# Kernel tuning notes

Hardware: AMD Instinct MI355X
Metric: run time of the kernel (lower is better)

The kernel has to match this reference:

```python
import jax, jax.numpy as jnp
import numpy as np

Q_MAX = 127.0  # int8 symmetric quant range


def setup_inputs() -> dict:
    key = jax.random.key(0)
    kx, kw, ks = jax.random.split(key, 3)
    M, K, N = 16384, 4096, 4096
    x = jax.random.normal(kx, (M, K), dtype=jnp.float32)
    # int8 weight values in [-127, 127]
    weight = jax.random.randint(kw, (N, K), -127, 128, dtype=jnp.int32).astype(jnp.int8)
    # per-output-row dequant scale, small positive values as a real quantizer would produce
    weight_scale = jax.random.uniform(ks, (N, 1), dtype=jnp.float32, minval=1e-3, maxval=1e-2)
    return {"x": x, "weight": weight, "weight_scale": weight_scale}


def reference(x, weight, weight_scale):
    # --- per-token dynamic activation quantization (get_hip_quant(per_Token)) ---
    amax = jnp.max(jnp.abs(x), axis=-1, keepdims=True)            # [M,1]
    x_scale = amax / Q_MAX                                        # [M,1]
    x_q = jnp.clip(jnp.round(x / jnp.maximum(x_scale, 1e-8)), -Q_MAX, Q_MAX)  # int8 values, kept fp32
    # --- gemm_a8w8: int8xint8 GEMM with fused dequant (row scale_a * col scale_b) ---
    acc = jnp.einsum('mk,nk->mn', x_q, weight.astype(jnp.float32),
                     preferred_element_type=jnp.float32)          # [M,N] int accumulation in fp32
    y = acc * x_scale * weight_scale.T                            # fused dequant scales
    return y  # fp32 stand-in for otype=bf16 output
```

## Files before the change

kernel.cpp:

```cpp
#include <hip/hip_runtime.h>
#include <stdint.h>

#define M_DIM 16384
#define N_DIM 4096
#define K_DIM 4096

#define BM 256
#define BN 256
#define BK 128
#define NT (K_DIM / BK)

typedef int i32x4 __attribute__((ext_vector_type(4)));

__device__ __forceinline__ void async16(const uint8_t* g, uint8_t* l) {
    __builtin_amdgcn_global_load_lds(
        (const __attribute__((address_space(1))) void*)g,
        (__attribute__((address_space(3))) void*)l,
        16, 0, 0);
}

__global__ __launch_bounds__(256) void pack_w_kernel(const int* __restrict__ w32,
                                                     uint32_t* __restrict__ w8,
                                                     int n4) {
    int i = blockIdx.x * 256 + threadIdx.x;
    if (i < n4) {
        const int4 v = reinterpret_cast<const int4*>(w32)[i];
        uint32_t p = (uint32_t)(v.x & 255) | ((uint32_t)(v.y & 255) << 8) |
                     ((uint32_t)(v.z & 255) << 16) | ((uint32_t)(v.w & 255) << 24);
        w8[i] = p;
    }
}

__global__ __launch_bounds__(256) void quant_kernel(const float* __restrict__ x,
                                                    uint32_t* __restrict__ xq,
                                                    float* __restrict__ xscale) {
    const int m = blockIdx.x;
    const int t = threadIdx.x;
    const float4* row = reinterpret_cast<const float4*>(x + (size_t)m * K_DIM);
    float4 v[4];
    float amax = 0.0f;
#pragma unroll
    for (int i = 0; i < 4; ++i) {
        v[i] = row[t + i * 256];
        amax = fmaxf(amax, fmaxf(fmaxf(fabsf(v[i].x), fabsf(v[i].y)),
                                 fmaxf(fabsf(v[i].z), fabsf(v[i].w))));
    }
#pragma unroll
    for (int off = 32; off > 0; off >>= 1) amax = fmaxf(amax, __shfl_xor(amax, off));
    __shared__ float smax[4];
    if ((t & 63) == 0) smax[t >> 6] = amax;
    __syncthreads();
    amax = fmaxf(fmaxf(smax[0], smax[1]), fmaxf(smax[2], smax[3]));
    const float scale = amax / 127.0f;
    const float s = fmaxf(scale, 1e-8f);
    if (t == 0) xscale[m] = scale;
    uint32_t* orow = xq + (size_t)m * (K_DIM / 4);
#pragma unroll
    for (int i = 0; i < 4; ++i) {
        int q0 = __float2int_rn(v[i].x / s);
        int q1 = __float2int_rn(v[i].y / s);
        int q2 = __float2int_rn(v[i].z / s);
        int q3 = __float2int_rn(v[i].w / s);
        q0 = max(-127, min(127, q0));
        q1 = max(-127, min(127, q1));
        q2 = max(-127, min(127, q2));
        q3 = max(-127, min(127, q3));
        uint32_t p = (uint32_t)(q0 & 255) | ((uint32_t)(q1 & 255) << 8) |
                     ((uint32_t)(q2 & 255) << 16) | ((uint32_t)(q3 & 255) << 24);
        orow[t + i * 256] = p;
    }
}

__global__ __launch_bounds__(512, 2) void gemm_kernel(
    const uint8_t* __restrict__ Aq, const float* __restrict__ ascale,
    const uint8_t* __restrict__ Bq, const float* __restrict__ wscale,
    float* __restrict__ out) {
    __shared__ uint8_t lds[2 * BM * BK + 2 * BN * BK];
    uint8_t* ldsA0 = lds;
    uint8_t* ldsA1 = lds + BM * BK;
    uint8_t* ldsB0 = lds + 2 * BM * BK;
    uint8_t* ldsB1 = lds + 2 * BM * BK + BN * BK;

    const int tid = threadIdx.x;
    const int lane = tid & 63;
    const int w = tid >> 6;
    const int wr = w >> 2;
    const int wc = w & 3;
    const int lr = lane & 15;
    const int lg = lane >> 4;
    const int aa = lane >> 3;
    const int pp = lane & 7;

    const int bid = blockIdx.x;
    const int swz = (bid & 7) * (1024 / 8) + (bid >> 3);
    const size_t row0 = (size_t)(swz >> 4) * BM;
    const size_t col0 = (size_t)(swz & 15) * BN;
    const uint8_t* Ab = Aq + row0 * K_DIM;
    const uint8_t* Bb = Bq + col0 * K_DIM;

    i32x4 acc[8][4];
#pragma unroll
    for (int i = 0; i < 8; ++i)
#pragma unroll
        for (int j = 0; j < 4; ++j) acc[i][j] = (i32x4){0, 0, 0, 0};

#define STAGE_A(DST, KT, MH)                                                     \
    do {                                                                         \
        _Pragma("unroll") for (int it_ = 0; it_ < 2; ++it_) {                    \
            const int m_ = (MH) * 64 + w * 8 + aa + it_ * 128;                   \
            async16(Ab + (size_t)m_ * K_DIM + (KT) * BK + ((pp ^ aa) << 4),      \
                    (DST) + ((MH) * 64 + w * 8 + it_ * 128) * BK);               \
        }                                                                        \
    } while (0)

#define STAGE_B(DST, KT, NH)                                                     \
    do {                                                                         \
        _Pragma("unroll") for (int it_ = 0; it_ < 2; ++it_) {                    \
            const int rwh_ = it_ * 64 + w * 8 + aa;                              \
            const int n_ = (NH) * 32 + (rwh_ & 31) + ((rwh_ >> 5) << 6);         \
            const int rw0_ = it_ * 64 + w * 8;                                   \
            const int nb_ = (NH) * 32 + (rw0_ & 31) + ((rw0_ >> 5) << 6);        \
            async16(Bb + (size_t)n_ * K_DIM + (KT) * BK + ((pp ^ aa) << 4),      \
                    (DST) + nb_ * BK);                                           \
        }                                                                        \
    } while (0)

#define READ_A(BUF, MH)                                                          \
    do {                                                                         \
        _Pragma("unroll") for (int mf_ = 0; mf_ < 4; ++mf_)                      \
        _Pragma("unroll") for (int kk_ = 0; kk_ < 2; ++kk_) {                    \
            const int r_ = wr * 128 + (MH) * 64 + mf_ * 16 + lr;                 \
            const int u_ = kk_ * 4 + lg;                                         \
            af[mf_][kk_] = *reinterpret_cast<const i32x4*>(                      \
                (BUF) + r_ * BK + ((u_ ^ (r_ & 7)) << 4));                       \
        }                                                                        \
    } while (0)

#define READ_B(BUF, NH, DSTF)                                                    \
    do {                                                                         \
        _Pragma("unroll") for (int nf_ = 0; nf_ < 2; ++nf_)                      \
        _Pragma("unroll") for (int kk_ = 0; kk_ < 2; ++kk_) {                    \
            const int r_ = wc * 64 + (NH) * 32 + nf_ * 16 + lr;                  \
            const int u_ = kk_ * 4 + lg;                                         \
            DSTF[nf_][kk_] = *reinterpret_cast<const i32x4*>(                    \
                (BUF) + r_ * BK + ((u_ ^ (r_ & 7)) << 4));                       \
        }                                                                        \
    } while (0)

#define MFMA_QUAD(MH, NH, BF)                                                    \
    do {                                                                         \
        __builtin_amdgcn_s_setprio(1);                                           \
        _Pragma("unroll") for (int mf_ = 0; mf_ < 4; ++mf_)                      \
        _Pragma("unroll") for (int nf_ = 0; nf_ < 2; ++nf_)                      \
        _Pragma("unroll") for (int kk_ = 0; kk_ < 2; ++kk_)                      \
            acc[(MH) * 4 + mf_][(NH) * 2 + nf_] =                                \
                __builtin_amdgcn_mfma_i32_16x16x64_i8(                           \
                    af[mf_][kk_], BF[nf_][kk_],                                  \
                    acc[(MH) * 4 + mf_][(NH) * 2 + nf_], 0, 0, 0);               \
        __builtin_amdgcn_s_setprio(0);                                           \
    } while (0)

#define BAR __builtin_amdgcn_s_barrier()
#define VMCNT6 asm volatile("s_waitcnt vmcnt(6)" ::: "memory")

    STAGE_A(ldsA0, 0, 0);
    STAGE_A(ldsA0, 0, 1);
    STAGE_B(ldsB0, 0, 0);
    STAGE_B(ldsB0, 0, 1);
    STAGE_A(ldsA1, 1, 0);
    STAGE_B(ldsB1, 1, 0);
    STAGE_B(ldsB1, 1, 1);
    VMCNT6;
    BAR;

    i32x4 af[4][2], bfA[2][2], bfB[2][2];

#pragma unroll 1
    for (int it2 = 0; it2 < NT / 2; ++it2) {
        const int t = 2 * it2;
        const int kt2 = (t + 2 < NT) ? t + 2 : NT - 1;
        const int kt3 = (t + 3 < NT) ? t + 3 : NT - 1;

        READ_A(ldsA0, 0);
        READ_B(ldsB0, 0, bfA);
        STAGE_A(ldsA1, t + 1, 1);
        BAR;
        MFMA_QUAD(0, 0, bfA);
        BAR;

        READ_B(ldsB0, 1, bfB);
        STAGE_A(ldsA0, kt2, 0);
        BAR;
        MFMA_QUAD(0, 1, bfB);
        BAR;

        READ_A(ldsA0, 1);
        STAGE_B(ldsB0, kt2, 0);
        BAR;
        MFMA_QUAD(1, 1, bfB);
        BAR;

        STAGE_B(ldsB0, kt2, 1);
        BAR;
        MFMA_QUAD(1, 0, bfA);
        VMCNT6;
        BAR;

        READ_A(ldsA1, 0);
        READ_B(ldsB1, 0, bfA);
        STAGE_A(ldsA0, kt2, 1);
        BAR;
        MFMA_QUAD(0, 0, bfA);
        BAR;

        READ_B(ldsB1, 1, bfB);
        STAGE_A(ldsA1, kt3, 0);
        BAR;
        MFMA_QUAD(0, 1, bfB);
        BAR;

        READ_A(ldsA1, 1);
        STAGE_B(ldsB1, kt3, 0);
        BAR;
        MFMA_QUAD(1, 1, bfB);
        BAR;

        STAGE_B(ldsB1, kt3, 1);
        BAR;
        MFMA_QUAD(1, 0, bfA);
        VMCNT6;
        BAR;
    }

    const float* asp = ascale + row0 + wr * 128;
    const float* wsp = wscale + col0 + wc * 64;
    float wsv[4];
#pragma unroll
    for (int nf = 0; nf < 4; ++nf) wsv[nf] = wsp[nf * 16 + lr];
    float* outBase = out + (row0 + wr * 128) * (size_t)N_DIM + col0 + wc * 64;
#pragma unroll
    for (int mf = 0; mf < 8; ++mf) {
#pragma unroll
        for (int j = 0; j < 4; ++j) {
            const int r = mf * 16 + lg * 4 + j;
            const float av = asp[r];
            float* orow = outBase + (size_t)r * N_DIM;
#pragma unroll
            for (int nf = 0; nf < 4; ++nf) {
                orow[nf * 16 + lr] = (float)acc[mf][nf][j] * av * wsv[nf];
            }
        }
    }
#undef STAGE_A
#undef STAGE_B
#undef READ_A
#undef READ_B
#undef MFMA_QUAD
#undef BAR
#undef VMCNT6
}

extern "C" void kernel_launch(void* const* d_in, const int* in_sizes, int n_in,
                              void* d_out, int out_size, void* d_ws, size_t ws_size,
                              hipStream_t stream) {
    const float* x = (const float*)d_in[0];
    const int* w32 = (const int*)d_in[1];
    const float* wscale = (const float*)d_in[2];
    float* out = (float*)d_out;

    uint8_t* ws = (uint8_t*)d_ws;
    uint32_t* xq = (uint32_t*)ws;
    float* xscale = (float*)(ws + (size_t)M_DIM * K_DIM);
    uint8_t* wq = ws + (size_t)M_DIM * K_DIM + (size_t)M_DIM * 4;

    pack_w_kernel<<<dim3((N_DIM * K_DIM / 4 + 255) / 256), 256, 0, stream>>>(
        w32, (uint32_t*)wq, N_DIM * K_DIM / 4);
    quant_kernel<<<dim3(M_DIM), 256, 0, stream>>>(x, xq, xscale);
    gemm_kernel<<<dim3((M_DIM / BM) * (N_DIM / BN)), 512, 0, stream>>>(
        (const uint8_t*)xq, xscale, wq, wscale, out);
}
```

Baseline: 346.5 us.

## Switch GEMM to 32x32x32 int8 MFMA and restructure per-tile schedule

Replaces the 16x16x64 int8 MFMA tiling with 32x32x32 int8 MFMA instructions, changing the accumulator layout to 16-element vectors and updating LDS fragment reads and the epilogue row mapping to match. The per-k-tile schedule is rearranged into fewer barrier phases, with explicit lgkmcnt waits and sched_barriers to overlap LDS reads with MFMA clusters. The vmcnt threshold is also adjusted to match the reordered prefetch. The larger MFMA shape cuts the number of LDS reads per FLOP and the instruction count. In exchange, the new wait counts and fragment mapping must stay correct, and fewer barriers may weaken the load/compute interleaving.

```diff
diff --git a/kernel.cpp b/kernel.cpp
--- a/kernel.cpp
+++ b/kernel.cpp
@@ -11,6 +11,7 @@
 #define NT (K_DIM / BK)
 
 typedef int i32x4 __attribute__((ext_vector_type(4)));
+typedef int i32x16 __attribute__((ext_vector_type(16)));
 
 __device__ __forceinline__ void async16(const uint8_t* g, uint8_t* l) {
     __builtin_amdgcn_global_load_lds(
@@ -86,8 +87,8 @@
     const int w = tid >> 6;
     const int wr = w >> 2;
     const int wc = w & 3;
-    const int lr = lane & 15;
-    const int lg = lane >> 4;
+    const int l31 = lane & 31;
+    const int hi = lane >> 5;
     const int aa = lane >> 3;
     const int pp = lane & 7;
 
@@ -98,11 +99,11 @@
     const uint8_t* Ab = Aq + row0 * K_DIM;
     const uint8_t* Bb = Bq + col0 * K_DIM;
 
-    i32x4 acc[8][4];
-#pragma unroll
-    for (int i = 0; i < 8; ++i)
-#pragma unroll
-        for (int j = 0; j < 4; ++j) acc[i][j] = (i32x4){0, 0, 0, 0};
+    i32x16 acc[4][2];
+#pragma unroll
+    for (int i = 0; i < 4; ++i)
+#pragma unroll
+        for (int j = 0; j < 2; ++j) acc[i][j] = (i32x16)(0);
 
 #define STAGE_A(DST, KT, MH)                                                     \
     do {                                                                         \
@@ -125,55 +126,66 @@
         }                                                                        \
     } while (0)
 
-#define READ_A(BUF, MH)                                                          \
-    do {                                                                         \
-        _Pragma("unroll") for (int mf_ = 0; mf_ < 4; ++mf_)                      \
-        _Pragma("unroll") for (int kk_ = 0; kk_ < 2; ++kk_) {                    \
-            const int r_ = wr * 128 + (MH) * 64 + mf_ * 16 + lr;                 \
-            const int u_ = kk_ * 4 + lg;                                         \
-            af[mf_][kk_] = *reinterpret_cast<const i32x4*>(                      \
+#define READ_A32(BUF, MH)                                                        \
+    do {                                                                         \
+        _Pragma("unroll") for (int mf_ = 0; mf_ < 2; ++mf_)                      \
+        _Pragma("unroll") for (int ks_ = 0; ks_ < 4; ++ks_) {                    \
+            const int r_ = wr * 128 + (MH) * 64 + mf_ * 32 + l31;                \
+            const int u_ = ks_ * 2 + hi;                                         \
+            af[mf_][ks_] = *reinterpret_cast<const i32x4*>(                      \
                 (BUF) + r_ * BK + ((u_ ^ (r_ & 7)) << 4));                       \
         }                                                                        \
     } while (0)
 
-#define READ_B(BUF, NH, DSTF)                                                    \
-    do {                                                                         \
-        _Pragma("unroll") for (int nf_ = 0; nf_ < 2; ++nf_)                      \
-        _Pragma("unroll") for (int kk_ = 0; kk_ < 2; ++kk_) {                    \
-            const int r_ = wc * 64 + (NH) * 32 + nf_ * 16 + lr;                  \
-            const int u_ = kk_ * 4 + lg;                                         \
-            DSTF[nf_][kk_] = *reinterpret_cast<const i32x4*>(                    \
+#define READ_B32(BUF, NH, DSTF)                                                  \
+    do {                                                                         \
+        _Pragma("unroll") for (int ks_ = 0; ks_ < 4; ++ks_) {                    \
+            const int r_ = wc * 64 + (NH) * 32 + l31;                            \
+            const int u_ = ks_ * 2 + hi;                                         \
+            DSTF[ks_] = *reinterpret_cast<const i32x4*>(                         \
                 (BUF) + r_ * BK + ((u_ ^ (r_ & 7)) << 4));                       \
         }                                                                        \
     } while (0)
 
-#define MFMA_QUAD(MH, NH, BF)                                                    \
+#define CLUSTER8(MH, NH, BF)                                                     \
     do {                                                                         \
         __builtin_amdgcn_s_setprio(1);                                           \
-        _Pragma("unroll") for (int mf_ = 0; mf_ < 4; ++mf_)                      \
-        _Pragma("unroll") for (int nf_ = 0; nf_ < 2; ++nf_)                      \
-        _Pragma("unroll") for (int kk_ = 0; kk_ < 2; ++kk_)                      \
-            acc[(MH) * 4 + mf_][(NH) * 2 + nf_] =                                \
-                __builtin_amdgcn_mfma_i32_16x16x64_i8(                           \
-                    af[mf_][kk_], BF[nf_][kk_],                                  \
-                    acc[(MH) * 4 + mf_][(NH) * 2 + nf_], 0, 0, 0);               \
+        _Pragma("unroll") for (int ks_ = 0; ks_ < 4; ++ks_)                      \
+        _Pragma("unroll") for (int mf_ = 0; mf_ < 2; ++mf_)                      \
+            acc[(MH) * 2 + mf_][NH] = __builtin_amdgcn_mfma_i32_32x32x32_i8(     \
+                af[mf_][ks_], BF[ks_], acc[(MH) * 2 + mf_][NH], 0, 0, 0);        \
         __builtin_amdgcn_s_setprio(0);                                           \
     } while (0)
 
+#define CLUSTER16(MH)                                                            \
+    do {                                                                         \
+        __builtin_amdgcn_s_setprio(1);                                           \
+        _Pragma("unroll") for (int ks_ = 0; ks_ < 4; ++ks_)                      \
+        _Pragma("unroll") for (int mf_ = 0; mf_ < 2; ++mf_) {                    \
+            acc[(MH) * 2 + mf_][1] = __builtin_amdgcn_mfma_i32_32x32x32_i8(      \
+                af[mf_][ks_], bf1[ks_], acc[(MH) * 2 + mf_][1], 0, 0, 0);        \
+            acc[(MH) * 2 + mf_][0] = __builtin_amdgcn_mfma_i32_32x32x32_i8(      \
+                af[mf_][ks_], bf0[ks_], acc[(MH) * 2 + mf_][0], 0, 0, 0);        \
+        }                                                                        \
+        __builtin_amdgcn_s_setprio(0);                                           \
+    } while (0)
+
 #define BAR __builtin_amdgcn_s_barrier()
-#define VMCNT6 asm volatile("s_waitcnt vmcnt(6)" ::: "memory")
+#define SB0 __builtin_amdgcn_sched_barrier(0)
+#define VMCNT8 asm volatile("s_waitcnt vmcnt(8)" ::: "memory")
+#define LGKM(N) asm volatile("s_waitcnt lgkmcnt(" #N ")" ::: "memory")
 
     STAGE_A(ldsA0, 0, 0);
-    STAGE_A(ldsA0, 0, 1);
     STAGE_B(ldsB0, 0, 0);
     STAGE_B(ldsB0, 0, 1);
+    STAGE_A(ldsA0, 0, 1);
     STAGE_A(ldsA1, 1, 0);
     STAGE_B(ldsB1, 1, 0);
     STAGE_B(ldsB1, 1, 1);
-    VMCNT6;
+    VMCNT8;
     BAR;
 
-    i32x4 af[4][2], bfA[2][2], bfB[2][2];
+    i32x4 af[2][4], bf0[4], bf1[4];
 
 #pragma unroll 1
     for (int it2 = 0; it2 < NT / 2; ++it2) {
@@ -181,83 +193,80 @@
         const int kt2 = (t + 2 < NT) ? t + 2 : NT - 1;
         const int kt3 = (t + 3 < NT) ? t + 3 : NT - 1;
 
-        READ_A(ldsA0, 0);
-        READ_B(ldsB0, 0, bfA);
+        READ_A32(ldsA0, 0);
+        READ_B32(ldsB0, 0, bf0);
+        SB0;
+        READ_B32(ldsB0, 1, bf1);
         STAGE_A(ldsA1, t + 1, 1);
         BAR;
-        MFMA_QUAD(0, 0, bfA);
-        BAR;
-
-        READ_B(ldsB0, 1, bfB);
+        LGKM(4);  SB0;
+        CLUSTER8(0, 0, bf0);
+        LGKM(0);  SB0;
+        CLUSTER8(0, 1, bf1);
+        VMCNT8;
+        BAR;
+        READ_A32(ldsA0, 1);
         STAGE_A(ldsA0, kt2, 0);
-        BAR;
-        MFMA_QUAD(0, 1, bfB);
-        BAR;
-
-        READ_A(ldsA0, 1);
         STAGE_B(ldsB0, kt2, 0);
-        BAR;
-        MFMA_QUAD(1, 1, bfB);
-        BAR;
-
         STAGE_B(ldsB0, kt2, 1);
         BAR;
-        MFMA_QUAD(1, 0, bfA);
-        VMCNT6;
-        BAR;
-
-        READ_A(ldsA1, 0);
-        READ_B(ldsB1, 0, bfA);
+        LGKM(0);  SB0;
+        CLUSTER16(1);
+        VMCNT8;
+        BAR;
+
+        READ_A32(ldsA1, 0);
+        READ_B32(ldsB1, 0, bf0);
+        SB0;
+        READ_B32(ldsB1, 1, bf1);
         STAGE_A(ldsA0, kt2, 1);
         BAR;
-        MFMA_QUAD(0, 0, bfA);
-        BAR;
-
-        READ_B(ldsB1, 1, bfB);
+        LGKM(4);  SB0;
+        CLUSTER8(0, 0, bf0);
+        LGKM(0);  SB0;
+        CLUSTER8(0, 1, bf1);
+        VMCNT8;
+        BAR;
+        READ_A32(ldsA1, 1);
         STAGE_A(ldsA1, kt3, 0);
-        BAR;
-        MFMA_QUAD(0, 1, bfB);
-        BAR;
-
-        READ_A(ldsA1, 1);
         STAGE_B(ldsB1, kt3, 0);
-        BAR;
-        MFMA_QUAD(1, 1, bfB);
-        BAR;
-
         STAGE_B(ldsB1, kt3, 1);
         BAR;
-        MFMA_QUAD(1, 0, bfA);
-        VMCNT6;
+        LGKM(0);  SB0;
+        CLUSTER16(1);
+        VMCNT8;
         BAR;
     }
 
     const float* asp = ascale + row0 + wr * 128;
     const float* wsp = wscale + col0 + wc * 64;
-    float wsv[4];
-#pragma unroll
-    for (int nf = 0; nf < 4; ++nf) wsv[nf] = wsp[nf * 16 + lr];
+    float wsv[2];
+#pragma unroll
+    for (int nf = 0; nf < 2; ++nf) wsv[nf] = wsp[nf * 32 + l31];
     float* outBase = out + (row0 + wr * 128) * (size_t)N_DIM + col0 + wc * 64;
 #pragma unroll
-    for (int mf = 0; mf < 8; ++mf) {
-#pragma unroll
-        for (int j = 0; j < 4; ++j) {
-            const int r = mf * 16 + lg * 4 + j;
+    for (int mf = 0; mf < 4; ++mf) {
+#pragma unroll
+        for (int j = 0; j < 16; ++j) {
+            const int r = mf * 32 + (j & 3) + 8 * (j >> 2) + 4 * hi;
             const float av = asp[r];
             float* orow = outBase + (size_t)r * N_DIM;
 #pragma unroll
-            for (int nf = 0; nf < 4; ++nf) {
-                orow[nf * 16 + lr] = (float)acc[mf][nf][j] * av * wsv[nf];
+            for (int nf = 0; nf < 2; ++nf) {
+                orow[nf * 32 + l31] = (float)acc[mf][nf][j] * av * wsv[nf];
             }
         }
     }
 #undef STAGE_A
 #undef STAGE_B
-#undef READ_A
-#undef READ_B
-#undef MFMA_QUAD
+#undef READ_A32
+#undef READ_B32
+#undef CLUSTER8
+#undef CLUSTER16
 #undef BAR
-#undef VMCNT6
+#undef SB0
+#undef VMCNT8
+#undef LGKM
 }
 
 extern "C" void kernel_launch(void* const* d_in, const int* in_sizes, int n_in,
```

Result: slower. 388.8 us (+12.2%).

## Restructure int8 GEMM main loop into k-split register double-buffered MFMA clusters

Applied to the files above, without the earlier changes.

Replaces the eight-phase quadrant schedule (many barriers, partial vmcnt waits) with a simpler pipeline. Each whole tile is staged to the other LDS buffer at once, and fragments are split along k into two register sets. The reads for the next k-half are issued while the current half's 32 MFMAs run. This cuts the number of barriers per tile and overlaps LDS reads with MFMA, but it holds more fragment registers live. It also waits with vmcnt(0) and lgkmcnt(0), which can expose global load latency and lower occupancy.

```diff
diff --git a/kernel.cpp b/kernel.cpp
--- a/kernel.cpp
+++ b/kernel.cpp
@@ -125,111 +125,89 @@
         }                                                                        \
     } while (0)
 
-#define READ_A(BUF, MH)                                                          \
-    do {                                                                         \
-        _Pragma("unroll") for (int mf_ = 0; mf_ < 4; ++mf_)                      \
-        _Pragma("unroll") for (int kk_ = 0; kk_ < 2; ++kk_) {                    \
-            const int r_ = wr * 128 + (MH) * 64 + mf_ * 16 + lr;                 \
-            const int u_ = kk_ * 4 + lg;                                         \
-            af[mf_][kk_] = *reinterpret_cast<const i32x4*>(                      \
+#define STAGE_TILE(LA, LB, KT)   \
+    do {                         \
+        STAGE_A(LA, KT, 0);      \
+        STAGE_A(LA, KT, 1);      \
+        STAGE_B(LB, KT, 0);      \
+        STAGE_B(LB, KT, 1);      \
+    } while (0)
+
+#define READ_AK(BUF, KK)                                                         \
+    do {                                                                         \
+        _Pragma("unroll") for (int q_ = 0; q_ < 8; ++q_) {                       \
+            const int r_ = wr * 128 + q_ * 16 + lr;                              \
+            const int u_ = (KK) * 4 + lg;                                        \
+            afk[KK][q_] = *reinterpret_cast<const i32x4*>(                       \
                 (BUF) + r_ * BK + ((u_ ^ (r_ & 7)) << 4));                       \
         }                                                                        \
     } while (0)
 
-#define READ_B(BUF, NH, DSTF)                                                    \
-    do {                                                                         \
-        _Pragma("unroll") for (int nf_ = 0; nf_ < 2; ++nf_)                      \
-        _Pragma("unroll") for (int kk_ = 0; kk_ < 2; ++kk_) {                    \
-            const int r_ = wc * 64 + (NH) * 32 + nf_ * 16 + lr;                  \
-            const int u_ = kk_ * 4 + lg;                                         \
-            DSTF[nf_][kk_] = *reinterpret_cast<const i32x4*>(                    \
+#define READ_BK(BUF, KK)                                                         \
+    do {                                                                         \
+        _Pragma("unroll") for (int p_ = 0; p_ < 4; ++p_) {                       \
+            const int r_ = wc * 64 + p_ * 16 + lr;                               \
+            const int u_ = (KK) * 4 + lg;                                        \
+            bfk[KK][p_] = *reinterpret_cast<const i32x4*>(                       \
                 (BUF) + r_ * BK + ((u_ ^ (r_ & 7)) << 4));                       \
         }                                                                        \
     } while (0)
 
-#define MFMA_QUAD(MH, NH, BF)                                                    \
+#define CLUSTER(KK)                                                              \
     do {                                                                         \
         __builtin_amdgcn_s_setprio(1);                                           \
-        _Pragma("unroll") for (int mf_ = 0; mf_ < 4; ++mf_)                      \
-        _Pragma("unroll") for (int nf_ = 0; nf_ < 2; ++nf_)                      \
-        _Pragma("unroll") for (int kk_ = 0; kk_ < 2; ++kk_)                      \
-            acc[(MH) * 4 + mf_][(NH) * 2 + nf_] =                                \
-                __builtin_amdgcn_mfma_i32_16x16x64_i8(                           \
-                    af[mf_][kk_], BF[nf_][kk_],                                  \
-                    acc[(MH) * 4 + mf_][(NH) * 2 + nf_], 0, 0, 0);               \
+        _Pragma("unroll") for (int q_ = 0; q_ < 8; ++q_)                         \
+        _Pragma("unroll") for (int p_ = 0; p_ < 4; ++p_)                         \
+            acc[q_][p_] = __builtin_amdgcn_mfma_i32_16x16x64_i8(                 \
+                afk[KK][q_], bfk[KK][p_], acc[q_][p_], 0, 0, 0);                 \
         __builtin_amdgcn_s_setprio(0);                                           \
     } while (0)
 
 #define BAR __builtin_amdgcn_s_barrier()
-#define VMCNT6 asm volatile("s_waitcnt vmcnt(6)" ::: "memory")
-
-    STAGE_A(ldsA0, 0, 0);
-    STAGE_A(ldsA0, 0, 1);
-    STAGE_B(ldsB0, 0, 0);
-    STAGE_B(ldsB0, 0, 1);
-    STAGE_A(ldsA1, 1, 0);
-    STAGE_B(ldsB1, 1, 0);
-    STAGE_B(ldsB1, 1, 1);
-    VMCNT6;
+#define SB0 __builtin_amdgcn_sched_barrier(0)
+#define VMCNT0 asm volatile("s_waitcnt vmcnt(0)" ::: "memory")
+#define LGKM0                                              \
+    do {                                                   \
+        asm volatile("s_waitcnt lgkmcnt(0)" ::: "memory"); \
+        __builtin_amdgcn_sched_barrier(0);                 \
+    } while (0)
+
+    i32x4 afk[2][8], bfk[2][4];
+
+    STAGE_TILE(ldsA0, ldsB0, 0);
+    VMCNT0;
     BAR;
-
-    i32x4 af[4][2], bfA[2][2], bfB[2][2];
+    READ_AK(ldsA0, 0);
+    READ_BK(ldsB0, 0);
 
 #pragma unroll 1
     for (int it2 = 0; it2 < NT / 2; ++it2) {
         const int t = 2 * it2;
-        const int kt2 = (t + 2 < NT) ? t + 2 : NT - 1;
-        const int kt3 = (t + 3 < NT) ? t + 3 : NT - 1;
-
-        READ_A(ldsA0, 0);
-        READ_B(ldsB0, 0, bfA);
-        STAGE_A(ldsA1, t + 1, 1);
+        const int tn2 = (t + 2 < NT) ? t + 2 : NT - 1;
+
+        LGKM0;
+        STAGE_TILE(ldsA1, ldsB1, t + 1);
+        READ_AK(ldsA0, 1);
+        READ_BK(ldsB0, 1);
+        CLUSTER(0);
+        LGKM0;
+        VMCNT0;
         BAR;
-        MFMA_QUAD(0, 0, bfA);
+        READ_AK(ldsA1, 0);
+        READ_BK(ldsB1, 0);
+        CLUSTER(1);
+
+        LGKM0;
+        STAGE_TILE(ldsA0, ldsB0, tn2);
+        READ_AK(ldsA1, 1);
+        READ_BK(ldsB1, 1);
+        CLUSTER(0);
+        LGKM0;
+        VMCNT0;
         BAR;
-
-        READ_B(ldsB0, 1, bfB);
-        STAGE_A(ldsA0, kt2, 0);
-        BAR;
-        MFMA_QUAD(0, 1, bfB);
-        BAR;
-
-        READ_A(ldsA0, 1);
-        STAGE_B(ldsB0, kt2, 0);
-        BAR;
-        MFMA_QUAD(1, 1, bfB);
-        BAR;
-
-        STAGE_B(ldsB0, kt2, 1);
-        BAR;
-        MFMA_QUAD(1, 0, bfA);
-        VMCNT6;
-        BAR;
-
-        READ_A(ldsA1, 0);
-        READ_B(ldsB1, 0, bfA);
-        STAGE_A(ldsA0, kt2, 1);
-        BAR;
-        MFMA_QUAD(0, 0, bfA);
-        BAR;
-
-        READ_B(ldsB1, 1, bfB);
-        STAGE_A(ldsA1, kt3, 0);
-        BAR;
-        MFMA_QUAD(0, 1, bfB);
-        BAR;
-
-        READ_A(ldsA1, 1);
-        STAGE_B(ldsB1, kt3, 0);
-        BAR;
-        MFMA_QUAD(1, 1, bfB);
-        BAR;
-
-        STAGE_B(ldsB1, kt3, 1);
-        BAR;
-        MFMA_QUAD(1, 0, bfA);
-        VMCNT6;
-        BAR;
+        READ_AK(ldsA0, 0);
+        READ_BK(ldsB0, 0);
+        CLUSTER(1);
     }
 
     const float* asp = ascale + row0 + wr * 128;
@@ -253,11 +231,14 @@
     }
 #undef STAGE_A
 #undef STAGE_B
-#undef READ_A
-#undef READ_B
-#undef MFMA_QUAD
+#undef STAGE_TILE
+#undef READ_AK
+#undef READ_BK
+#undef CLUSTER
 #undef BAR
-#undef VMCNT6
+#undef SB0
+#undef VMCNT0
+#undef LGKM0
 }
 
 extern "C" void kernel_launch(void* const* d_in, const int* in_sizes, int n_in,
```

Result: slower. 558.5 us (+61.2%).
